# Kernel tuning notes

Measured on AMD Instinct MI355X. Metric: run time of the kernel, lower is better.

The kernel has to match this reference:

```python
import jax, jax.numpy as jnp
import numpy as np

WINDOW = 12
NUM_HEADS = 16

def window_partition(x, ws):
    b, h, w, c = x.shape
    x = x.reshape(b, h // ws, ws, w // ws, ws, c)
    return x.transpose(0, 1, 3, 2, 4, 5).reshape(-1, ws, ws, c)

def window_reverse(windows, ws, h, w):
    c = windows.shape[-1]
    x = windows.reshape(-1, h // ws, w // ws, ws, ws, c)
    return x.transpose(0, 1, 3, 2, 4, 5).reshape(-1, h, w, c)

def setup_inputs() -> dict:
    key = jax.random.key(0)
    ks = jax.random.split(key, 5)
    dim = 512
    hidden_states = jax.random.normal(ks[0], (8, 48, 48, dim), dtype=jnp.float32)
    qkv_w = jax.random.normal(ks[1], (dim, 3 * dim), dtype=jnp.float32) * 0.02
    qkv_b = jnp.zeros((3 * dim,), dtype=jnp.float32)
    proj_w = jax.random.normal(ks[2], (dim, dim), dtype=jnp.float32) * 0.02
    proj_b = jnp.zeros((dim,), dtype=jnp.float32)
    return {"hidden_states": hidden_states, "qkv_w": qkv_w, "qkv_b": qkv_b,
            "proj_w": proj_w, "proj_b": proj_b}

def reference(hidden_states, qkv_w, qkv_b, proj_w, proj_b):
    b, h, w, c = hidden_states.shape
    ws = WINDOW
    nh = NUM_HEADS
    hd = c // nh
    scale = hd ** -0.5
    pad_r = (ws - w % ws) % ws
    pad_b = (ws - h % ws) % ws
    x = jnp.pad(hidden_states, ((0, 0), (0, pad_b), (0, pad_r), (0, 0)))
    ph, pw = x.shape[1], x.shape[2]
    # [nW, ws*ws, C]
    xw = window_partition(x, ws).reshape(-1, ws * ws, c)
    nw, nt, _ = xw.shape
    qkv = (xw @ qkv_w + qkv_b).reshape(nw, nt, 3, nh, hd)
    qkv = qkv.transpose(2, 0, 3, 1, 4)  # [3, nW, nh, nt, hd]
    q, k, v = qkv[0], qkv[1], qkv[2]
    scores = jnp.einsum('wnqd,wnkd->wnqk', q, k) * scale
    attn = jax.nn.softmax(scores, axis=-1)
    out = jnp.einsum('wnqk,wnkd->wnqd', attn, v)  # [nW, nh, nt, hd]
    out = out.transpose(0, 2, 1, 3).reshape(nw, nt, c)
    out = out @ proj_w + proj_b
    out = out.reshape(-1, ws, ws, c)
    out = window_reverse(out, ws, ph, pw)
    out = out[:, :h, :w, :]
    return out.reshape(b, h * w, c)
```

## Files before the change

### kernel.cpp

```cpp
#include <hip/hip_runtime.h>
#include <hip/hip_bf16.h>


typedef unsigned short u16;
typedef unsigned int u32;
typedef __attribute__((ext_vector_type(4))) float f32x4;
typedef __attribute__((ext_vector_type(8))) short short8;

#define MFMA16(a, b, c) __builtin_amdgcn_mfma_f32_16x16x32_bf16(a, b, c, 0, 0, 0)

__device__ __forceinline__ u16 f2b(float f) {
  __hip_bfloat16 h = __float2bfloat16(f);
  return *reinterpret_cast<u16*>(&h);
}

__global__ void prep_x_kernel(const float* __restrict__ x, u16* __restrict__ xw) {
  int c = blockIdx.x * 256 + threadIdx.x;
  int r = c >> 6;
  int colb = (c & 63) << 3;
  int win = r / 144, tok = r - win * 144;
  int b = win >> 4, wh = (win >> 2) & 3, ww = win & 3;
  int i = tok / 12, j = tok - i * 12;
  const float* src = x + ((size_t)((b * 48 + wh * 12 + i) * 48 + ww * 12 + j)) * 512 + colb;
  float4 a0 = *(const float4*)(src);
  float4 a1 = *(const float4*)(src + 4);
  short8 o;
  o[0] = (short)f2b(a0.x); o[1] = (short)f2b(a0.y); o[2] = (short)f2b(a0.z); o[3] = (short)f2b(a0.w);
  o[4] = (short)f2b(a1.x); o[5] = (short)f2b(a1.y); o[6] = (short)f2b(a1.z); o[7] = (short)f2b(a1.w);
  *reinterpret_cast<short8*>(xw + (size_t)r * 512 + colb) = o;
}

__global__ void prep_wt_kernel(const float* __restrict__ w, u16* __restrict__ wt,
                               int K, int N) {
  int t = blockIdx.x * 256 + threadIdx.x;
  int nchunks = N >> 3;
  if (t >= K * nchunks) return;
  int k = t / nchunks;
  int n0 = (t - k * nchunks) << 3;
  const float* src = w + (size_t)k * N + n0;
  float4 a0 = *(const float4*)(src);
  float4 a1 = *(const float4*)(src + 4);
  float v[8] = {a0.x, a0.y, a0.z, a0.w, a1.x, a1.y, a1.z, a1.w};
#pragma unroll
  for (int j = 0; j < 8; j++) wt[(size_t)(n0 + j) * K + k] = f2b(v[j]);
}

template <int EPI>
__global__ __launch_bounds__(256) void gemm_bt_kernel(
    const u16* __restrict__ A, const u16* __restrict__ BT,
    const float* __restrict__ bias,
    u16* __restrict__ outb, float* __restrict__ outf,
    int M, int N, int K) {
  __shared__ __align__(16) u16 sA[128 * 64];
  __shared__ __align__(16) u16 sB[128 * 64];
  const int tid = threadIdx.x;
  const int wave = tid >> 6;
  const int lane = tid & 63;
  const int bm = blockIdx.x;
  const int bn = blockIdx.y;
  const int wr = (wave >> 1) << 6;
  const int wc = (wave & 1) << 6;
  const int l15 = lane & 15;
  const int lhi = lane >> 4;

  f32x4 acc[4][4];
  const f32x4 fzero = {0.f, 0.f, 0.f, 0.f};
#pragma unroll
  for (int i = 0; i < 4; i++)
#pragma unroll
    for (int j = 0; j < 4; j++) acc[i][j] = fzero;

  const int srow = lane >> 3;
  const int scol = (((lane & 7) ^ srow) << 3);
  const u16* Abase = A + (size_t)(bm * 128) * K;
  const u16* Bbase = BT + (size_t)(bn * 128) * K;

  for (int k0 = 0; k0 < K; k0 += 64) {
#pragma unroll
    for (int i = 0; i < 4; ++i) {
      const int chunk = wave * 4 + i;
      const int row = chunk * 8 + srow;
      __builtin_amdgcn_global_load_lds(
          (const __attribute__((address_space(1))) u32*)(Abase + (size_t)row * K + k0 + scol),
          (__attribute__((address_space(3))) u32*)(sA + chunk * 512), 16, 0, 0);
      __builtin_amdgcn_global_load_lds(
          (const __attribute__((address_space(1))) u32*)(Bbase + (size_t)row * K + k0 + scol),
          (__attribute__((address_space(3))) u32*)(sB + chunk * 512), 16, 0, 0);
    }
    __syncthreads();

    short8 af[4][2], bfr[4][2];
#pragma unroll
    for (int t = 0; t < 4; t++) {
#pragma unroll
      for (int kk = 0; kk < 2; kk++) {
        const int rA = wr + t * 16 + l15;
        const int rB = wc + t * 16 + l15;
        const int cA = (kk * 32 + lhi * 8) ^ ((rA & 7) << 3);
        const int cB = (kk * 32 + lhi * 8) ^ ((rB & 7) << 3);
        af[t][kk]  = *reinterpret_cast<const short8*>(sA + rA * 64 + cA);
        bfr[t][kk] = *reinterpret_cast<const short8*>(sB + rB * 64 + cB);
      }
    }
#pragma unroll
    for (int kk = 0; kk < 2; kk++)
#pragma unroll
      for (int i = 0; i < 4; i++)
#pragma unroll
        for (int j = 0; j < 4; j++)
          acc[i][j] = MFMA16(af[i][kk], bfr[j][kk], acc[i][j]);
    __syncthreads();
  }

#pragma unroll
  for (int i = 0; i < 4; i++) {
    const int rowbase = bm * 128 + wr + i * 16 + lhi * 4;
#pragma unroll
    for (int j = 0; j < 4; j++) {
      const int col = bn * 128 + wc + j * 16 + l15;
      const float bv = bias[col];
#pragma unroll
      for (int r = 0; r < 4; r++) {
        float v = acc[i][j][r] + bv;
        int row = rowbase + r;
        if (EPI == 0) {
          outb[(size_t)row * N + col] = f2b(v);
        } else {
          int win = row / 144, tok = row - win * 144;
          int b = win >> 4, wh = (win >> 2) & 3, ww = win & 3;
          int ii = tok / 12, jj = tok - ii * 12;
          size_t o = ((size_t)b * 2304 + (wh * 12 + ii) * 48 + (ww * 12 + jj)) * 512 + col;
          outf[o] = v;
        }
      }
    }
  }
}

__global__ __launch_bounds__(192) void attn_kernel(const u16* __restrict__ qkv,
                                                   u16* __restrict__ outb) {
  constexpr int PSTR = 168;
  __shared__ __align__(16) u16 sVT[32 * PSTR];
  __shared__ __align__(16) u16 sP[3 * 16 * PSTR];
  const int tid = threadIdx.x;
  const int wave = tid >> 6;
  const int lane = tid & 63;
  const int l15 = lane & 15;
  const int lhi = lane >> 4;
  const int win = blockIdx.x;
  const int head = blockIdx.y;
  const size_t base = ((size_t)win * 144) * 1536 + head * 32;
  const u16* Q = qkv + base;
  const u16* Kp = qkv + base + 512;
  const u16* V = qkv + base + 1024;
  constexpr float SC2 = 0.25509915922608635f;
  const f32x4 fzero = {0.f, 0.f, 0.f, 0.f};

  for (int t = tid; t < 576; t += 192) {
    int tok = t >> 2, dblk = t & 3;
    short8 v = *reinterpret_cast<const short8*>(V + (size_t)tok * 1536 + dblk * 8);
#pragma unroll
    for (int j = 0; j < 8; j++) sVT[(dblk * 8 + j) * PSTR + tok] = (u16)v[j];
  }
  for (int t = tid; t < 512; t += 192) {
    int d = t >> 4, cc = 144 + (t & 15);
    sVT[d * PSTR + cc] = 0;
  }
  u16* sPw = sP + wave * 16 * PSTR;
  {
    for (int t = lane; t < 256; t += 64) {
      int rr = t >> 4, cc = 144 + (t & 15);
      sPw[rr * PSTR + cc] = 0;
    }
  }

  short8 qa[3];
#pragma unroll
  for (int mt = 0; mt < 3; mt++) {
    int row = wave * 48 + mt * 16 + l15;
    qa[mt] = *reinterpret_cast<const short8*>(Q + (size_t)row * 1536 + lhi * 8);
  }
  short8 kb[9];
#pragma unroll
  for (int nt = 0; nt < 9; nt++) {
    int ctok = nt * 16 + l15;
    kb[nt] = *reinterpret_cast<const short8*>(Kp + (size_t)ctok * 1536 + lhi * 8);
  }

  __syncthreads();

  f32x4 o[3][2];
#pragma unroll
  for (int mt = 0; mt < 3; mt++)
#pragma unroll
    for (int nt = 0; nt < 2; nt++) o[mt][nt] = fzero;

#pragma unroll
  for (int mt = 0; mt < 3; mt++) {
    f32x4 s[9];
#pragma unroll
    for (int nt = 0; nt < 9; nt++) s[nt] = MFMA16(qa[mt], kb[nt], fzero);

#pragma unroll
    for (int r = 0; r < 4; r++) {
      float m = -1e30f;
#pragma unroll
      for (int nt = 0; nt < 9; nt++) m = fmaxf(m, s[nt][r]);
#pragma unroll
      for (int off = 1; off < 16; off <<= 1) m = fmaxf(m, __shfl_xor(m, off, 64));
      float p[9], sum = 0.f;
#pragma unroll
      for (int nt = 0; nt < 9; nt++) {
        p[nt] = exp2f((s[nt][r] - m) * SC2);
        sum += p[nt];
      }
#pragma unroll
      for (int off = 1; off < 16; off <<= 1) sum += __shfl_xor(sum, off, 64);
      float inv = 1.f / sum;
      int prow = lhi * 4 + r;
#pragma unroll
      for (int nt = 0; nt < 9; nt++)
        sPw[prow * PSTR + nt * 16 + l15] = f2b(p[nt] * inv);
    }

#pragma unroll
    for (int kk = 0; kk < 5; kk++) {
      short8 pa = *reinterpret_cast<const short8*>(sPw + l15 * PSTR + kk * 32 + lhi * 8);
#pragma unroll
      for (int nt = 0; nt < 2; nt++) {
        short8 vb = *reinterpret_cast<const short8*>(sVT + (nt * 16 + l15) * PSTR + kk * 32 + lhi * 8);
        o[mt][nt] = MFMA16(pa, vb, o[mt][nt]);
      }
    }
  }

  const int rowb = win * 144 + wave * 48;
#pragma unroll
  for (int mt = 0; mt < 3; mt++) {
#pragma unroll
    for (int nt = 0; nt < 2; nt++) {
      int col = head * 32 + nt * 16 + l15;
#pragma unroll
      for (int r = 0; r < 4; r++) {
        int row = rowb + mt * 16 + lhi * 4 + r;
        outb[(size_t)row * 512 + col] = f2b(o[mt][nt][r]);
      }
    }
  }
}

extern "C" void kernel_launch(void* const* d_in, const int* in_sizes, int n_in,
                              void* d_out, int out_size, void* d_ws, size_t ws_size,
                              hipStream_t stream) {
  const float* x      = (const float*)d_in[0];
  const float* qkv_w  = (const float*)d_in[1];
  const float* qkv_b  = (const float*)d_in[2];
  const float* proj_w = (const float*)d_in[3];
  const float* proj_b = (const float*)d_in[4];
  float* out = (float*)d_out;

  u16* xw     = (u16*)d_ws;
  u16* qkvT   = xw + (size_t)18432 * 512;
  u16* projT  = qkvT + (size_t)1536 * 512;
  u16* qkvout = projT + (size_t)512 * 512;
  u16* attno  = qkvout + (size_t)18432 * 1536;

  prep_x_kernel<<<4608, 256, 0, stream>>>(x, xw);
  prep_wt_kernel<<<384, 256, 0, stream>>>(qkv_w, qkvT, 512, 1536);
  prep_wt_kernel<<<128, 256, 0, stream>>>(proj_w, projT, 512, 512);

  gemm_bt_kernel<0><<<dim3(144, 12), 256, 0, stream>>>(
      xw, qkvT, qkv_b, qkvout, nullptr, 18432, 1536, 512);

  attn_kernel<<<dim3(128, 16), 192, 0, stream>>>(qkvout, attno);

  gemm_bt_kernel<1><<<dim3(144, 4), 256, 0, stream>>>(
      attno, projT, proj_b, nullptr, out, 18432, 512, 512);
}
```

Before: 209.7 us.

## Use 256x256 GEMM tiles with triple-buffered LDS and async prefetch

Replaces the 128x128, 256-thread GEMM with a 256x256-tile, 512-thread kernel. It triple-buffers LDS over K-steps of 32, issuing global_load_lds prefetches two stages ahead, and interleaves them with MFMA work using explicit vmcnt waits and raised priority around the MFMAs. The aim is to hide global-load latency behind compute and raise data reuse per tile. The cost is fewer blocks: the projection GEMM gets only 144 blocks on a 256-CU part, and each thread needs more accumulator registers.

```diff
diff --git a/kernel.cpp b/kernel.cpp
--- a/kernel.cpp
+++ b/kernel.cpp
@@ -8,6 +8,8 @@
 typedef __attribute__((ext_vector_type(8))) short short8;
 
 #define MFMA16(a, b, c) __builtin_amdgcn_mfma_f32_16x16x32_bf16(a, b, c, 0, 0, 0)
+#define AS1 __attribute__((address_space(1)))
+#define AS3 __attribute__((address_space(3)))
 
 __device__ __forceinline__ u16 f2b(float f) {
   __hip_bfloat16 h = __float2bfloat16(f);
@@ -46,83 +48,114 @@
 }
 
 template <int EPI>
-__global__ __launch_bounds__(256) void gemm_bt_kernel(
+__global__ __launch_bounds__(512, 2) void gemm256_kernel(
     const u16* __restrict__ A, const u16* __restrict__ BT,
     const float* __restrict__ bias,
     u16* __restrict__ outb, float* __restrict__ outf,
     int M, int N, int K) {
-  __shared__ __align__(16) u16 sA[128 * 64];
-  __shared__ __align__(16) u16 sB[128 * 64];
+  __shared__ __align__(16) u16 sA[3][8192];
+  __shared__ __align__(16) u16 sB[3][8192];
   const int tid = threadIdx.x;
   const int wave = tid >> 6;
   const int lane = tid & 63;
-  const int bm = blockIdx.x;
-  const int bn = blockIdx.y;
-  const int wr = (wave >> 1) << 6;
-  const int wc = (wave & 1) << 6;
+  const int wr = wave >> 2;
+  const int wc = wave & 3;
   const int l15 = lane & 15;
   const int lhi = lane >> 4;
-
-  f32x4 acc[4][4];
+  const int bm = blockIdx.x, bn = blockIdx.y;
+
+  f32x4 acc[8][4];
   const f32x4 fzero = {0.f, 0.f, 0.f, 0.f};
 #pragma unroll
-  for (int i = 0; i < 4; i++)
+  for (int i = 0; i < 8; i++)
 #pragma unroll
     for (int j = 0; j < 4; j++) acc[i][j] = fzero;
 
-  const int srow = lane >> 3;
-  const int scol = (((lane & 7) ^ srow) << 3);
-  const u16* Abase = A + (size_t)(bm * 128) * K;
-  const u16* Bbase = BT + (size_t)(bn * 128) * K;
-
-  for (int k0 = 0; k0 < K; k0 += 64) {
-#pragma unroll
-    for (int i = 0; i < 4; ++i) {
-      const int chunk = wave * 4 + i;
-      const int row = chunk * 8 + srow;
+  const int srow = lane >> 2;
+  const int scol = (((lane & 3) ^ ((lane >> 3) & 3)) << 3);
+  const int rcol = ((lhi ^ ((l15 >> 1) & 3)) << 3);
+
+  const u16* Ab = A + (size_t)(bm * 256) * K;
+  const u16* Bb = BT + (size_t)(bn * 256) * K;
+  const int nt = K >> 5;
+
+#pragma unroll
+  for (int t0 = 0; t0 < 2; ++t0) {
+    const int k0 = t0 << 5;
+#pragma unroll
+    for (int h = 0; h < 2; ++h) {
+      const int c = wave * 2 + h;
       __builtin_amdgcn_global_load_lds(
-          (const __attribute__((address_space(1))) u32*)(Abase + (size_t)row * K + k0 + scol),
-          (__attribute__((address_space(3))) u32*)(sA + chunk * 512), 16, 0, 0);
+          (const AS1 u32*)(Ab + (size_t)(c * 16 + srow) * K + k0 + scol),
+          (AS3 u32*)(&sA[t0][c * 512]), 16, 0, 0);
+    }
+#pragma unroll
+    for (int h = 0; h < 2; ++h) {
+      const int c = wave * 2 + h;
       __builtin_amdgcn_global_load_lds(
-          (const __attribute__((address_space(1))) u32*)(Bbase + (size_t)row * K + k0 + scol),
-          (__attribute__((address_space(3))) u32*)(sB + chunk * 512), 16, 0, 0);
-    }
-    __syncthreads();
-
-    short8 af[4][2], bfr[4][2];
-#pragma unroll
-    for (int t = 0; t < 4; t++) {
-#pragma unroll
-      for (int kk = 0; kk < 2; kk++) {
-        const int rA = wr + t * 16 + l15;
-        const int rB = wc + t * 16 + l15;
-        const int cA = (kk * 32 + lhi * 8) ^ ((rA & 7) << 3);
-        const int cB = (kk * 32 + lhi * 8) ^ ((rB & 7) << 3);
-        af[t][kk]  = *reinterpret_cast<const short8*>(sA + rA * 64 + cA);
-        bfr[t][kk] = *reinterpret_cast<const short8*>(sB + rB * 64 + cB);
-      }
-    }
-#pragma unroll
-    for (int kk = 0; kk < 2; kk++)
-#pragma unroll
-      for (int i = 0; i < 4; i++)
-#pragma unroll
-        for (int j = 0; j < 4; j++)
-          acc[i][j] = MFMA16(af[i][kk], bfr[j][kk], acc[i][j]);
-    __syncthreads();
-  }
-
-#pragma unroll
-  for (int i = 0; i < 4; i++) {
-    const int rowbase = bm * 128 + wr + i * 16 + lhi * 4;
-#pragma unroll
-    for (int j = 0; j < 4; j++) {
-      const int col = bn * 128 + wc + j * 16 + l15;
+          (const AS1 u32*)(Bb + (size_t)(c * 16 + srow) * K + k0 + scol),
+          (AS3 u32*)(&sB[t0][c * 512]), 16, 0, 0);
+    }
+  }
+
+  for (int t = 0; t < nt; ++t) {
+    const int cur = t % 3;
+    const bool has2 = (t + 2 < nt);
+    const int nxt = (t + 2) % 3;
+    const int k2 = (t + 2) << 5;
+
+    if (t + 1 < nt) { asm volatile("s_waitcnt vmcnt(4)"); }
+    else           { asm volatile("s_waitcnt vmcnt(0)"); }
+    __builtin_amdgcn_sched_barrier(0);
+    __builtin_amdgcn_s_barrier();
+    __builtin_amdgcn_sched_barrier(0);
+
+    const u16* pA = &sA[cur][0];
+    const u16* pB = &sB[cur][0];
+    short8 bf[4];
+#pragma unroll
+    for (int p = 0; p < 4; ++p) {
+      if (has2) {
+        const int c = wave * 2 + (p & 1);
+        if (p < 2)
+          __builtin_amdgcn_global_load_lds(
+              (const AS1 u32*)(Ab + (size_t)(c * 16 + srow) * K + k2 + scol),
+              (AS3 u32*)(&sA[nxt][c * 512]), 16, 0, 0);
+        else
+          __builtin_amdgcn_global_load_lds(
+              (const AS1 u32*)(Bb + (size_t)(c * 16 + srow) * K + k2 + scol),
+              (AS3 u32*)(&sB[nxt][c * 512]), 16, 0, 0);
+      }
+      short8 a0 = *reinterpret_cast<const short8*>(pA + (wr * 128 + (2 * p) * 16 + l15) * 32 + rcol);
+      short8 a1 = *reinterpret_cast<const short8*>(pA + (wr * 128 + (2 * p + 1) * 16 + l15) * 32 + rcol);
+      if (p == 0) {
+#pragma unroll
+        for (int n = 0; n < 4; ++n)
+          bf[n] = *reinterpret_cast<const short8*>(pB + (wc * 64 + n * 16 + l15) * 32 + rcol);
+      }
+      __builtin_amdgcn_s_setprio(1);
+#pragma unroll
+      for (int n = 0; n < 4; ++n) {
+        acc[2 * p][n]     = MFMA16(a0, bf[n], acc[2 * p][n]);
+        acc[2 * p + 1][n] = MFMA16(a1, bf[n], acc[2 * p + 1][n]);
+      }
+      __builtin_amdgcn_s_setprio(0);
+    }
+    __builtin_amdgcn_sched_barrier(0);
+    __builtin_amdgcn_s_barrier();
+  }
+
+#pragma unroll
+  for (int i = 0; i < 8; ++i) {
+    const int row0 = bm * 256 + wr * 128 + i * 16 + lhi * 4;
+#pragma unroll
+    for (int j = 0; j < 4; ++j) {
+      const int col = bn * 256 + wc * 64 + j * 16 + l15;
       const float bv = bias[col];
 #pragma unroll
-      for (int r = 0; r < 4; r++) {
+      for (int r = 0; r < 4; ++r) {
         float v = acc[i][j][r] + bv;
-        int row = rowbase + r;
+        const int row = row0 + r;
         if (EPI == 0) {
           outb[(size_t)row * N + col] = f2b(v);
         } else {
@@ -269,11 +302,11 @@
   prep_wt_kernel<<<384, 256, 0, stream>>>(qkv_w, qkvT, 512, 1536);
   prep_wt_kernel<<<128, 256, 0, stream>>>(proj_w, projT, 512, 512);
 
-  gemm_bt_kernel<0><<<dim3(144, 12), 256, 0, stream>>>(
+  gemm256_kernel<0><<<dim3(72, 6), 512, 0, stream>>>(
       xw, qkvT, qkv_b, qkvout, nullptr, 18432, 1536, 512);
 
   attn_kernel<<<dim3(128, 16), 192, 0, stream>>>(qkvout, attno);
 
-  gemm_bt_kernel<1><<<dim3(144, 4), 256, 0, stream>>>(
+  gemm256_kernel<1><<<dim3(72, 2), 512, 0, stream>>>(
       attno, projT, proj_b, nullptr, out, 18432, 512, 512);
 }
```

Result: no change. 209.9 us (+0.1%).
